# Kernel tuning notes

Hardware: AMD Instinct MI355X
Metric: run time of the kernel (lower is better)

Reference implementation:

```python
import jax, jax.numpy as jnp
import numpy as np

NUM_CLASSES = 10000
FEATURE_DIM = 512
BATCH = 16384


def setup_inputs() -> dict:
    key = jax.random.key(0)
    k1, k2, k3 = jax.random.split(key, 3)
    feat = jax.random.normal(k1, (BATCH, FEATURE_DIM), dtype=jnp.float32)
    label = jax.random.randint(k2, (BATCH,), 0, NUM_CLASSES, dtype=jnp.int32)
    centers = jax.random.normal(k3, (NUM_CLASSES, FEATURE_DIM), dtype=jnp.float32)
    return {"feat": feat, "label": label, "centers": centers}


def reference(feat, label, centers):
    # Gather per-sample class centers: [B, D]
    centers_exp = centers[label]
    # torch.histc(label, bins=C, min=0, max=C) with unit-width bins == per-class bincount
    count = jnp.zeros((NUM_CLASSES,), dtype=jnp.float32).at[label].add(1.0)
    num = count[label]  # [B]
    dist = jnp.sqrt(jnp.sum((feat - centers_exp) ** 2, axis=1))  # [B]
    loss = jnp.sum(dist / num) / feat.shape[0]
    return loss
```

## Files before the change

kernel.cpp:

```cpp
#include <hip/hip_runtime.h>


constexpr int NUM_CLASSES = 10000;
constexpr int FEATURE_DIM = 512;
constexpr int BATCH       = 16384;

constexpr int HIST_BLOCKS    = 40;
constexpr int BINS_PER_BLOCK = NUM_CLASSES / HIST_BLOCKS;

constexpr int DIST_THREADS      = 512;
constexpr int WAVES_PER_BLOCK   = DIST_THREADS / 64;
constexpr int SAMPLES_PER_WAVE  = 4;
constexpr int SAMPLES_PER_BLOCK = WAVES_PER_BLOCK * SAMPLES_PER_WAVE;
constexpr int DIST_BLOCKS       = BATCH / SAMPLES_PER_BLOCK;

typedef float vfloat4 __attribute__((ext_vector_type(4)));
typedef int   vint4   __attribute__((ext_vector_type(4)));

__global__ __launch_bounds__(1024) void center_hist_kernel(const int* __restrict__ label,
                                                           int* __restrict__ count,
                                                           float* __restrict__ out) {
    __shared__ int h[BINS_PER_BLOCK];
    const int lo = blockIdx.x * BINS_PER_BLOCK;

    for (int i = threadIdx.x; i < BINS_PER_BLOCK; i += 1024) h[i] = 0;
    __syncthreads();

    const vint4* lab4 = reinterpret_cast<const vint4*>(label);
    for (int i = threadIdx.x; i < BATCH / 4; i += 1024) {
        const vint4 l = lab4[i];
        int a;
        a = l.x - lo; if ((unsigned)a < (unsigned)BINS_PER_BLOCK) atomicAdd(&h[a], 1);
        a = l.y - lo; if ((unsigned)a < (unsigned)BINS_PER_BLOCK) atomicAdd(&h[a], 1);
        a = l.z - lo; if ((unsigned)a < (unsigned)BINS_PER_BLOCK) atomicAdd(&h[a], 1);
        a = l.w - lo; if ((unsigned)a < (unsigned)BINS_PER_BLOCK) atomicAdd(&h[a], 1);
    }
    __syncthreads();

    for (int i = threadIdx.x; i < BINS_PER_BLOCK; i += 1024) count[lo + i] = h[i];

    if (blockIdx.x == 0 && threadIdx.x == 0) out[0] = 0.0f;
}

__device__ __forceinline__ float sq8(vfloat4 fa, vfloat4 fb, vfloat4 ca, vfloat4 cb) {
    vfloat4 da = fa - ca, db = fb - cb;
    return da.x*da.x + da.y*da.y + da.z*da.z + da.w*da.w
         + db.x*db.x + db.y*db.y + db.z*db.z + db.w*db.w;
}

__global__ __launch_bounds__(DIST_THREADS, 4) void center_dist_kernel(const float* __restrict__ feat,
                                                                      const int* __restrict__ label,
                                                                      const float* __restrict__ centers,
                                                                      const int* __restrict__ count,
                                                                      float* __restrict__ out) {
    __shared__ float wave_part[WAVES_PER_BLOCK];
    const int wave = threadIdx.x >> 6;
    const int lane = threadIdx.x & 63;

    const int b = __builtin_amdgcn_readfirstlane(
        blockIdx.x * SAMPLES_PER_BLOCK + wave * SAMPLES_PER_WAVE);

    const int lab0 = label[b + 0];
    const int lab1 = label[b + 1];
    const int lab2 = label[b + 2];
    const int lab3 = label[b + 3];
    const int cnt0 = count[lab0];
    const int cnt1 = count[lab1];
    const int cnt2 = count[lab2];
    const int cnt3 = count[lab3];

    const vfloat4* f0 = reinterpret_cast<const vfloat4*>(feat + (size_t)(b + 0) * FEATURE_DIM);
    const vfloat4* f1 = reinterpret_cast<const vfloat4*>(feat + (size_t)(b + 1) * FEATURE_DIM);
    const vfloat4* f2 = reinterpret_cast<const vfloat4*>(feat + (size_t)(b + 2) * FEATURE_DIM);
    const vfloat4* f3 = reinterpret_cast<const vfloat4*>(feat + (size_t)(b + 3) * FEATURE_DIM);
    const vfloat4* c0 = reinterpret_cast<const vfloat4*>(centers + (size_t)lab0 * FEATURE_DIM);
    const vfloat4* c1 = reinterpret_cast<const vfloat4*>(centers + (size_t)lab1 * FEATURE_DIM);
    const vfloat4* c2 = reinterpret_cast<const vfloat4*>(centers + (size_t)lab2 * FEATURE_DIM);
    const vfloat4* c3 = reinterpret_cast<const vfloat4*>(centers + (size_t)lab3 * FEATURE_DIM);

    vfloat4 fa0 = f0[lane], fb0 = f0[lane + 64];
    vfloat4 fa1 = f1[lane], fb1 = f1[lane + 64];
    vfloat4 fa2 = f2[lane], fb2 = f2[lane + 64];
    vfloat4 fa3 = f3[lane], fb3 = f3[lane + 64];
    vfloat4 ca0 = c0[lane], cb0 = c0[lane + 64];
    vfloat4 ca1 = c1[lane], cb1 = c1[lane + 64];
    vfloat4 ca2 = c2[lane], cb2 = c2[lane + 64];
    vfloat4 ca3 = c3[lane], cb3 = c3[lane + 64];

    float s0 = sq8(fa0, fb0, ca0, cb0);
    float s1 = sq8(fa1, fb1, ca1, cb1);
    float s2 = sq8(fa2, fb2, ca2, cb2);
    float s3 = sq8(fa3, fb3, ca3, cb3);

    #pragma unroll
    for (int off = 32; off > 0; off >>= 1) {
        s0 += __shfl_down(s0, off, 64);
        s1 += __shfl_down(s1, off, 64);
        s2 += __shfl_down(s2, off, 64);
        s3 += __shfl_down(s3, off, 64);
    }

    if (lane == 0) {
        wave_part[wave] = sqrtf(s0) / (float)cnt0
                        + sqrtf(s1) / (float)cnt1
                        + sqrtf(s2) / (float)cnt2
                        + sqrtf(s3) / (float)cnt3;
    }
    __syncthreads();

    if (threadIdx.x == 0) {
        float sum = 0.0f;
        #pragma unroll
        for (int w = 0; w < WAVES_PER_BLOCK; ++w) sum += wave_part[w];
        atomicAdd(out, sum * (1.0f / (float)BATCH));
    }
}

extern "C" void kernel_launch(void* const* d_in, const int* in_sizes, int n_in,
                              void* d_out, int out_size, void* d_ws, size_t ws_size,
                              hipStream_t stream) {
    const float* feat    = (const float*)d_in[0];
    const int*   label   = (const int*)  d_in[1];
    const float* centers = (const float*)d_in[2];
    float*       out     = (float*)d_out;
    int*         count   = (int*)d_ws;

    center_hist_kernel<<<HIST_BLOCKS, 1024, 0, stream>>>(label, count, out);

    center_dist_kernel<<<DIST_BLOCKS, DIST_THREADS, 0, stream>>>(
        feat, label, centers, count, out);
}
```

Measured before the change: 95.48 us.

## Fuse histogram and distance kernels into one cooperative launch with grid sync

Merges the per-class histogram kernel and the distance/reduction kernel into a single cooperatively launched kernel. The first 40 blocks build the class histogram, then a grid-wide barrier is taken before every block computes its distances. The aim is to remove the second kernel launch and the gap between the two kernels. In exchange, the histogram phase now runs with 512 threads per block instead of 1024, every block stalls at the grid barrier, and cooperative launch adds its own overhead and requires all blocks to be co-resident.

```diff
diff --git a/kernel.cpp b/kernel.cpp
--- a/kernel.cpp
+++ b/kernel.cpp
@@ -1,46 +1,24 @@
 #include <hip/hip_runtime.h>
+#include <hip/hip_cooperative_groups.h>
+
+namespace cg = cooperative_groups;
 
 
 constexpr int NUM_CLASSES = 10000;
 constexpr int FEATURE_DIM = 512;
 constexpr int BATCH       = 16384;
 
-constexpr int HIST_BLOCKS    = 40;
-constexpr int BINS_PER_BLOCK = NUM_CLASSES / HIST_BLOCKS;
-
-constexpr int DIST_THREADS      = 512;
-constexpr int WAVES_PER_BLOCK   = DIST_THREADS / 64;
+constexpr int THREADS           = 512;
+constexpr int WAVES_PER_BLOCK   = THREADS / 64;
 constexpr int SAMPLES_PER_WAVE  = 4;
 constexpr int SAMPLES_PER_BLOCK = WAVES_PER_BLOCK * SAMPLES_PER_WAVE;
-constexpr int DIST_BLOCKS       = BATCH / SAMPLES_PER_BLOCK;
+constexpr int BLOCKS            = BATCH / SAMPLES_PER_BLOCK;
+
+constexpr int HIST_ACTIVE    = 40;
+constexpr int BINS_PER_BLOCK = NUM_CLASSES / HIST_ACTIVE;
 
 typedef float vfloat4 __attribute__((ext_vector_type(4)));
 typedef int   vint4   __attribute__((ext_vector_type(4)));
-
-__global__ __launch_bounds__(1024) void center_hist_kernel(const int* __restrict__ label,
-                                                           int* __restrict__ count,
-                                                           float* __restrict__ out) {
-    __shared__ int h[BINS_PER_BLOCK];
-    const int lo = blockIdx.x * BINS_PER_BLOCK;
-
-    for (int i = threadIdx.x; i < BINS_PER_BLOCK; i += 1024) h[i] = 0;
-    __syncthreads();
-
-    const vint4* lab4 = reinterpret_cast<const vint4*>(label);
-    for (int i = threadIdx.x; i < BATCH / 4; i += 1024) {
-        const vint4 l = lab4[i];
-        int a;
-        a = l.x - lo; if ((unsigned)a < (unsigned)BINS_PER_BLOCK) atomicAdd(&h[a], 1);
-        a = l.y - lo; if ((unsigned)a < (unsigned)BINS_PER_BLOCK) atomicAdd(&h[a], 1);
-        a = l.z - lo; if ((unsigned)a < (unsigned)BINS_PER_BLOCK) atomicAdd(&h[a], 1);
-        a = l.w - lo; if ((unsigned)a < (unsigned)BINS_PER_BLOCK) atomicAdd(&h[a], 1);
-    }
-    __syncthreads();
-
-    for (int i = threadIdx.x; i < BINS_PER_BLOCK; i += 1024) count[lo + i] = h[i];
-
-    if (blockIdx.x == 0 && threadIdx.x == 0) out[0] = 0.0f;
-}
 
 __device__ __forceinline__ float sq8(vfloat4 fa, vfloat4 fb, vfloat4 ca, vfloat4 cb) {
     vfloat4 da = fa - ca, db = fb - cb;
@@ -48,12 +26,40 @@
          + db.x*db.x + db.y*db.y + db.z*db.z + db.w*db.w;
 }
 
-__global__ __launch_bounds__(DIST_THREADS, 4) void center_dist_kernel(const float* __restrict__ feat,
-                                                                      const int* __restrict__ label,
-                                                                      const float* __restrict__ centers,
-                                                                      const int* __restrict__ count,
-                                                                      float* __restrict__ out) {
+__global__ __launch_bounds__(THREADS, 4) void center_fused_kernel(const float* __restrict__ feat,
+                                                                  const int* __restrict__ label,
+                                                                  const float* __restrict__ centers,
+                                                                  int* __restrict__ count,
+                                                                  float* __restrict__ out) {
+    __shared__ int   h[BINS_PER_BLOCK];
     __shared__ float wave_part[WAVES_PER_BLOCK];
+
+    cg::grid_group grid = cg::this_grid();
+
+    if (blockIdx.x < HIST_ACTIVE) {
+        const int lo = blockIdx.x * BINS_PER_BLOCK;
+
+        for (int i = threadIdx.x; i < BINS_PER_BLOCK; i += THREADS) h[i] = 0;
+        __syncthreads();
+
+        const vint4* lab4 = reinterpret_cast<const vint4*>(label);
+        for (int i = threadIdx.x; i < BATCH / 4; i += THREADS) {
+            const vint4 l = lab4[i];
+            int a;
+            a = l.x - lo; if ((unsigned)a < (unsigned)BINS_PER_BLOCK) atomicAdd(&h[a], 1);
+            a = l.y - lo; if ((unsigned)a < (unsigned)BINS_PER_BLOCK) atomicAdd(&h[a], 1);
+            a = l.z - lo; if ((unsigned)a < (unsigned)BINS_PER_BLOCK) atomicAdd(&h[a], 1);
+            a = l.w - lo; if ((unsigned)a < (unsigned)BINS_PER_BLOCK) atomicAdd(&h[a], 1);
+        }
+        __syncthreads();
+
+        for (int i = threadIdx.x; i < BINS_PER_BLOCK; i += THREADS) count[lo + i] = h[i];
+
+        if (blockIdx.x == 0 && threadIdx.x == 0) out[0] = 0.0f;
+    }
+
+    grid.sync();
+
     const int wave = threadIdx.x >> 6;
     const int lane = threadIdx.x & 63;
 
@@ -125,8 +131,8 @@
     float*       out     = (float*)d_out;
     int*         count   = (int*)d_ws;
 
-    center_hist_kernel<<<HIST_BLOCKS, 1024, 0, stream>>>(label, count, out);
-
-    center_dist_kernel<<<DIST_BLOCKS, DIST_THREADS, 0, stream>>>(
-        feat, label, centers, count, out);
+    void* args[] = {(void*)&feat, (void*)&label, (void*)&centers,
+                    (void*)&count, (void*)&out};
+    hipLaunchCooperativeKernel((const void*)center_fused_kernel,
+                               dim3(BLOCKS), dim3(THREADS), args, 0, stream);
 }
```

Measured after the change: 155.7 us. +63.1%, slower.
